# Optimization experiments

Hardware: AMD Instinct MI355X
Metric: run time of the kernel (lower is better)

The kernel has to match this reference:

```python
import jax, jax.numpy as jnp
import numpy as np

UNITS = 1024
NUM_HEADS = 16
MASK_VALUE = -1e12


def setup_inputs() -> dict:
    key = jax.random.key(0)
    k1, k2, k3, k4 = jax.random.split(key, 4)
    B, S = 8, 1024
    memory = jax.random.normal(k1, (B, S, 2 * UNITS), dtype=jnp.float32)
    query = jax.random.normal(k2, (B, S, UNITS), dtype=jnp.float32)
    b = jax.random.normal(k3, (S,), dtype=jnp.float32)
    seq_len = jax.random.randint(k4, (B, 1), 0, S, dtype=jnp.int32)
    return {"memory": memory, "query": query, "b": b, "seq_len": seq_len}


def _split_heads(x, n):
    # [B, S, D] -> [B, n, S, D/n]
    B, S, D = x.shape
    return x.reshape(B, S, n, D // n).transpose(0, 2, 1, 3)


def reference(memory, query, b, seq_len):
    B, S, _ = query.shape
    dh = UNITS // NUM_HEADS
    k_mem, v_mem = jnp.split(memory, 2, axis=2)
    Q = _split_heads(query, NUM_HEADS) * (dh ** -0.5)   # [B,H,S,dh]
    Kh = _split_heads(k_mem, NUM_HEADS)                  # [B,H,S,dh]
    Vh = _split_heads(v_mem, NUM_HEADS)                  # [B,H,S,dh]
    logits = jnp.einsum('bhqd,bhkd->bhqk', Q, Kh) + b    # bias broadcast over keys
    # mask: one_hot(seq_len) -> cumsum -> 1-cumsum == (pos < seq_len)
    valid = (jnp.arange(S)[None, :] < seq_len[:, 0:1]).astype(jnp.float32)  # [B,S]
    logits = logits + MASK_VALUE * (1.0 - valid)[:, None, None, :]
    weights = jax.nn.softmax(logits, axis=-1)
    out = jnp.einsum('bhqk,bhkd->bhqd', weights, Vh)
    return out.transpose(0, 2, 1, 3).reshape(B, S, UNITS)
```

## Files before the change

kernel.cpp:

```cpp
#include <hip/hip_runtime.h>
#include <hip/hip_bf16.h>

#define B_      8
#define S_      1024
#define H_      16
#define DH      64
#define UNITS_  1024
#define MSTRIDE 2048
#define KVB     64
#define QTB     64
#define LP      72

typedef __attribute__((ext_vector_type(8))) short bf16x8;
typedef __attribute__((ext_vector_type(4))) float f32x4;

__device__ __forceinline__ unsigned short f2bf(float f) {
    union { float f; unsigned u; } x; x.f = f;
    unsigned r = x.u + 0x7fffu + ((x.u >> 16) & 1u);
    return (unsigned short)(r >> 16);
}

__global__ __launch_bounds__(256)
void attn_kernel(const float* __restrict__ mem, const float* __restrict__ qry,
                 const float* __restrict__ bias, const int* __restrict__ slen,
                 float* __restrict__ out)
{
    __shared__ alignas(16) unsigned short Qs[QTB][LP];
    __shared__ alignas(16) unsigned short Ks[KVB][LP];
    __shared__ alignas(16) unsigned short Vt[DH][LP];
    __shared__ alignas(16) unsigned short Ps[4][16][LP];

    const int tid  = threadIdx.x;
    const int wq   = tid >> 6;
    const int lane = tid & 63;
    const int lr   = lane & 15;
    const int lg   = lane >> 4;

    const int qt = blockIdx.x;
    const int h  = blockIdx.y;
    const int b  = blockIdx.z;

    int L = slen[b];
    if (L == 0) L = S_;
    const int ntiles = (L + KVB - 1) / KVB;

    const float* qp = qry + ((size_t)(b * S_ + qt * QTB)) * UNITS_ + h * DH;
    const float* kp = mem + ((size_t)b * S_) * MSTRIDE + h * DH;
    const float* vp = kp + UNITS_;
    float*       op = out + ((size_t)(b * S_ + qt * QTB)) * UNITS_ + h * DH;

    {
        const int row = tid >> 2;
        const int cb  = (tid & 3) * 16;
        const float4* src = (const float4*)(qp + (size_t)row * UNITS_ + cb);
        union { unsigned short us[16]; uint4 v[2]; } t;
        #pragma unroll
        for (int i = 0; i < 4; ++i) {
            float4 f = src[i];
            t.us[i*4+0] = f2bf(f.x * 0.125f);
            t.us[i*4+1] = f2bf(f.y * 0.125f);
            t.us[i*4+2] = f2bf(f.z * 0.125f);
            t.us[i*4+3] = f2bf(f.w * 0.125f);
        }
        uint4* d = (uint4*)&Qs[row][cb];
        d[0] = t.v[0]; d[1] = t.v[1];
    }
    __syncthreads();

    bf16x8 qf[2];
    #pragma unroll
    for (int kc = 0; kc < 2; ++kc)
        qf[kc] = *(const bf16x8*)&Qs[wq*16 + lr][kc*32 + lg*8];

    f32x4 o[4];
    float m[4], ls[4];
    #pragma unroll
    for (int r = 0; r < 4; ++r) {
        o[r] = (f32x4){0.f,0.f,0.f,0.f};
        m[r] = -INFINITY; ls[r] = 0.f;
    }

    for (int t = 0; t < ntiles; ++t) {
        const int kvb = t * KVB;
        {
            const int row = tid >> 2;
            const int cb  = (tid & 3) * 16;
            const float4* ks = (const float4*)(kp + (size_t)(kvb + row) * MSTRIDE + cb);
            union { unsigned short us[16]; uint4 v[2]; } tk;
            #pragma unroll
            for (int i = 0; i < 4; ++i) {
                float4 f = ks[i];
                tk.us[i*4+0] = f2bf(f.x); tk.us[i*4+1] = f2bf(f.y);
                tk.us[i*4+2] = f2bf(f.z); tk.us[i*4+3] = f2bf(f.w);
            }
            uint4* d = (uint4*)&Ks[row][cb];
            d[0] = tk.v[0]; d[1] = tk.v[1];
            const float4* vs = (const float4*)(vp + (size_t)(kvb + row) * MSTRIDE + cb);
            #pragma unroll
            for (int i = 0; i < 4; ++i) {
                float4 f = vs[i];
                Vt[cb + i*4 + 0][row] = f2bf(f.x);
                Vt[cb + i*4 + 1][row] = f2bf(f.y);
                Vt[cb + i*4 + 2][row] = f2bf(f.z);
                Vt[cb + i*4 + 3][row] = f2bf(f.w);
            }
        }
        __syncthreads();

        f32x4 s[4];
        #pragma unroll
        for (int cb = 0; cb < 4; ++cb) {
            f32x4 acc = (f32x4){0.f,0.f,0.f,0.f};
            #pragma unroll
            for (int kc = 0; kc < 2; ++kc) {
                bf16x8 kf = *(const bf16x8*)&Ks[cb*16 + lr][kc*32 + lg*8];
                acc = __builtin_amdgcn_mfma_f32_16x16x32_bf16(qf[kc], kf, acc, 0, 0, 0);
            }
            s[cb] = acc;
        }

        float p[4][4];
        float rowm[4] = {-INFINITY, -INFINITY, -INFINITY, -INFINITY};
        #pragma unroll
        for (int cb = 0; cb < 4; ++cb) {
            const int key = kvb + cb*16 + lr;
            const float bb = bias[key];
            const bool valid = key < L;
            #pragma unroll
            for (int r = 0; r < 4; ++r) {
                float v = valid ? (s[cb][r] + bb) : -INFINITY;
                p[cb][r] = v;
                rowm[r] = fmaxf(rowm[r], v);
            }
        }
        #pragma unroll
        for (int off = 1; off < 16; off <<= 1) {
            #pragma unroll
            for (int r = 0; r < 4; ++r)
                rowm[r] = fmaxf(rowm[r], __shfl_xor(rowm[r], off, 64));
        }
        float sc[4], rs[4];
        #pragma unroll
        for (int r = 0; r < 4; ++r) {
            float mnew = fmaxf(m[r], rowm[r]);
            sc[r] = __expf(m[r] - mnew);
            m[r] = mnew;
            float acc = 0.f;
            #pragma unroll
            for (int cb = 0; cb < 4; ++cb) {
                float e = __expf(p[cb][r] - mnew);
                p[cb][r] = e;
                acc += e;
            }
            rs[r] = acc;
        }
        #pragma unroll
        for (int off = 1; off < 16; off <<= 1) {
            #pragma unroll
            for (int r = 0; r < 4; ++r)
                rs[r] += __shfl_xor(rs[r], off, 64);
        }
        #pragma unroll
        for (int r = 0; r < 4; ++r) {
            ls[r] = ls[r] * sc[r] + rs[r];
            #pragma unroll
            for (int c = 0; c < 4; ++c)
                o[c][r] *= sc[r];
        }

        #pragma unroll
        for (int cb = 0; cb < 4; ++cb)
            #pragma unroll
            for (int r = 0; r < 4; ++r)
                Ps[wq][lg*4 + r][cb*16 + lr] = f2bf(p[cb][r]);
        asm volatile("s_waitcnt lgkmcnt(0)" ::: "memory");

        #pragma unroll
        for (int kc = 0; kc < 2; ++kc) {
            bf16x8 pf = *(const bf16x8*)&Ps[wq][lr][kc*32 + lg*8];
            #pragma unroll
            for (int c = 0; c < 4; ++c) {
                bf16x8 vf = *(const bf16x8*)&Vt[c*16 + lr][kc*32 + lg*8];
                o[c] = __builtin_amdgcn_mfma_f32_16x16x32_bf16(pf, vf, o[c], 0, 0, 0);
            }
        }
        __syncthreads();
    }

    #pragma unroll
    for (int r = 0; r < 4; ++r) {
        const float inv = 1.0f / ls[r];
        float* orow = op + (size_t)(wq*16 + lg*4 + r) * UNITS_;
        #pragma unroll
        for (int c = 0; c < 4; ++c)
            orow[c*16 + lr] = o[c][r] * inv;
    }
}

extern "C" void kernel_launch(void* const* d_in, const int* in_sizes, int n_in,
                              void* d_out, int out_size, void* d_ws, size_t ws_size,
                              hipStream_t stream) {
    const float* mem  = (const float*)d_in[0];
    const float* qry  = (const float*)d_in[1];
    const float* bias = (const float*)d_in[2];
    const int*   slen = (const int*)d_in[3];
    float*       out  = (float*)d_out;
    dim3 grid(S_ / QTB, H_, B_);
    attn_kernel<<<grid, dim3(256), 0, stream>>>(mem, qry, bias, slen, out);
}
```

Before: 193.5 us.

## Double query rows per block, drop running max, use transposed LDS reads for V

```diff
diff --git a/kernel.cpp b/kernel.cpp
--- a/kernel.cpp
+++ b/kernel.cpp
@@ -1,5 +1,4 @@
 #include <hip/hip_runtime.h>
-#include <hip/hip_bf16.h>
 
 #define B_      8
 #define S_      1024
@@ -8,26 +7,27 @@
 #define UNITS_  1024
 #define MSTRIDE 2048
 #define KVB     64
-#define QTB     64
+#define QTB     128
 #define LP      72
+#define LOG2E   1.4426950408889634f
 
 typedef __attribute__((ext_vector_type(8))) short bf16x8;
+typedef __attribute__((ext_vector_type(4))) short bf16x4;
 typedef __attribute__((ext_vector_type(4))) float f32x4;
 
-__device__ __forceinline__ unsigned short f2bf(float f) {
-    union { float f; unsigned u; } x; x.f = f;
-    unsigned r = x.u + 0x7fffu + ((x.u >> 16) & 1u);
-    return (unsigned short)(r >> 16);
+__device__ __forceinline__ unsigned cvt_pk_bf16(float lo, float hi) {
+    unsigned r;
+    asm("v_cvt_pk_bf16_f32 %0, %1, %2" : "=v"(r) : "v"(lo), "v"(hi));
+    return r;
 }
 
-__global__ __launch_bounds__(256)
+__global__ __launch_bounds__(256, 4)
 void attn_kernel(const float* __restrict__ mem, const float* __restrict__ qry,
                  const float* __restrict__ bias, const int* __restrict__ slen,
                  float* __restrict__ out)
 {
-    __shared__ alignas(16) unsigned short Qs[QTB][LP];
     __shared__ alignas(16) unsigned short Ks[KVB][LP];
-    __shared__ alignas(16) unsigned short Vt[DH][LP];
+    __shared__ alignas(16) unsigned short Vs[KVB * DH];
     __shared__ alignas(16) unsigned short Ps[4][16][LP];
 
     const int tid  = threadIdx.x;
@@ -49,152 +49,143 @@
     const float* vp = kp + UNITS_;
     float*       op = out + ((size_t)(b * S_ + qt * QTB)) * UNITS_ + h * DH;
 
-    {
-        const int row = tid >> 2;
-        const int cb  = (tid & 3) * 16;
-        const float4* src = (const float4*)(qp + (size_t)row * UNITS_ + cb);
-        union { unsigned short us[16]; uint4 v[2]; } t;
-        #pragma unroll
-        for (int i = 0; i < 4; ++i) {
-            float4 f = src[i];
-            t.us[i*4+0] = f2bf(f.x * 0.125f);
-            t.us[i*4+1] = f2bf(f.y * 0.125f);
-            t.us[i*4+2] = f2bf(f.z * 0.125f);
-            t.us[i*4+3] = f2bf(f.w * 0.125f);
-        }
-        uint4* d = (uint4*)&Qs[row][cb];
-        d[0] = t.v[0]; d[1] = t.v[1];
-    }
-    __syncthreads();
-
-    bf16x8 qf[2];
+    bf16x8 qf[2][2];
     #pragma unroll
-    for (int kc = 0; kc < 2; ++kc)
-        qf[kc] = *(const bf16x8*)&Qs[wq*16 + lr][kc*32 + lg*8];
-
-    f32x4 o[4];
-    float m[4], ls[4];
+    for (int rb = 0; rb < 2; ++rb)
+      #pragma unroll
+      for (int kc = 0; kc < 2; ++kc) {
+        const float* qrow = qp + (size_t)(wq*32 + rb*16 + lr) * UNITS_ + kc*32 + lg*8;
+        float4 f0 = ((const float4*)qrow)[0];
+        float4 f1 = ((const float4*)qrow)[1];
+        const float sc = 0.125f * LOG2E;
+        uint4 u;
+        u.x = cvt_pk_bf16(f0.x*sc, f0.y*sc);
+        u.y = cvt_pk_bf16(f0.z*sc, f0.w*sc);
+        u.z = cvt_pk_bf16(f1.x*sc, f1.y*sc);
+        u.w = cvt_pk_bf16(f1.z*sc, f1.w*sc);
+        qf[rb][kc] = __builtin_bit_cast(bf16x8, u);
+      }
+
+    f32x4 o[2][4];
+    float ls[2][4];
     #pragma unroll
-    for (int r = 0; r < 4; ++r) {
-        o[r] = (f32x4){0.f,0.f,0.f,0.f};
-        m[r] = -INFINITY; ls[r] = 0.f;
-    }
+    for (int rb = 0; rb < 2; ++rb)
+      #pragma unroll
+      for (int r = 0; r < 4; ++r) {
+        o[rb][r] = (f32x4){0.f,0.f,0.f,0.f};
+        ls[rb][r] = 0.f;
+      }
+
+    const unsigned vsb = (unsigned)(uintptr_t)&Vs[0];
+    const int krow = tid >> 2;
+    const int dblk = tid & 3;
 
     for (int t = 0; t < ntiles; ++t) {
         const int kvb = t * KVB;
         {
-            const int row = tid >> 2;
-            const int cb  = (tid & 3) * 16;
-            const float4* ks = (const float4*)(kp + (size_t)(kvb + row) * MSTRIDE + cb);
-            union { unsigned short us[16]; uint4 v[2]; } tk;
+            const float4* ks = (const float4*)(kp + (size_t)(kvb + krow) * MSTRIDE + dblk * 16);
+            float4 a0 = ks[0], a1 = ks[1], a2 = ks[2], a3 = ks[3];
+            uint4 w0, w1;
+            w0.x = cvt_pk_bf16(a0.x, a0.y); w0.y = cvt_pk_bf16(a0.z, a0.w);
+            w0.z = cvt_pk_bf16(a1.x, a1.y); w0.w = cvt_pk_bf16(a1.z, a1.w);
+            w1.x = cvt_pk_bf16(a2.x, a2.y); w1.y = cvt_pk_bf16(a2.z, a2.w);
+            w1.z = cvt_pk_bf16(a3.x, a3.y); w1.w = cvt_pk_bf16(a3.z, a3.w);
+            uint4* d = (uint4*)&Ks[krow][dblk * 16];
+            d[0] = w0; d[1] = w1;
+        }
+        {
+            const float* vr = vp + (size_t)(kvb + krow) * MSTRIDE;
             #pragma unroll
             for (int i = 0; i < 4; ++i) {
-                float4 f = ks[i];
-                tk.us[i*4+0] = f2bf(f.x); tk.us[i*4+1] = f2bf(f.y);
-                tk.us[i*4+2] = f2bf(f.z); tk.us[i*4+3] = f2bf(f.w);
+                const int rot = (i + (krow >> 2)) & 3;
+                const int d0  = dblk * 16 + rot * 4;
+                float4 f = *(const float4*)(vr + d0);
+                uint2 w;
+                w.x = cvt_pk_bf16(f.x, f.y);
+                w.y = cvt_pk_bf16(f.z, f.w);
+                const int e = ((krow >> 2) << 8) + ((d0 >> 4) << 6) + ((krow & 3) << 4) + (d0 & 15);
+                *(uint2*)&Vs[e] = w;
             }
-            uint4* d = (uint4*)&Ks[row][cb];
-            d[0] = tk.v[0]; d[1] = tk.v[1];
-            const float4* vs = (const float4*)(vp + (size_t)(kvb + row) * MSTRIDE + cb);
-            #pragma unroll
-            for (int i = 0; i < 4; ++i) {
-                float4 f = vs[i];
-                Vt[cb + i*4 + 0][row] = f2bf(f.x);
-                Vt[cb + i*4 + 1][row] = f2bf(f.y);
-                Vt[cb + i*4 + 2][row] = f2bf(f.z);
-                Vt[cb + i*4 + 3][row] = f2bf(f.w);
+        }
+        __syncthreads();
+
+        float bv[4];
+        #pragma unroll
+        for (int cb = 0; cb < 4; ++cb) {
+            const int key = kvb + cb * 16 + lr;
+            bv[cb] = (key < L) ? bias[key] * LOG2E : -INFINITY;
+        }
+
+        bf16x4 vt[2][4][2];
+        #pragma unroll
+        for (int kc = 0; kc < 2; ++kc)
+          #pragma unroll
+          for (int c = 0; c < 4; ++c) {
+            unsigned a1 = vsb + ((kc * 8 + lg * 2) << 9) + (c << 7) + (lr << 3);
+            asm volatile("ds_read_b64_tr_b16 %0, %1" : "=v"(vt[kc][c][0]) : "v"(a1));
+            asm volatile("ds_read_b64_tr_b16 %0, %1 offset:512" : "=v"(vt[kc][c][1]) : "v"(a1));
+          }
+
+        #pragma unroll
+        for (int rb = 0; rb < 2; ++rb) {
+            f32x4 s[4];
+            #pragma unroll
+            for (int cb = 0; cb < 4; ++cb) {
+                f32x4 acc = (f32x4){0.f,0.f,0.f,0.f};
+                #pragma unroll
+                for (int kc = 0; kc < 2; ++kc) {
+                    bf16x8 kf = *(const bf16x8*)&Ks[cb * 16 + lr][kc * 32 + lg * 8];
+                    acc = __builtin_amdgcn_mfma_f32_16x16x32_bf16(qf[rb][kc], kf, acc, 0, 0, 0);
+                }
+                s[cb] = acc;
             }
-        }
-        __syncthreads();
-
-        f32x4 s[4];
-        #pragma unroll
-        for (int cb = 0; cb < 4; ++cb) {
-            f32x4 acc = (f32x4){0.f,0.f,0.f,0.f};
+            #pragma unroll
+            for (int cb = 0; cb < 4; ++cb)
+                #pragma unroll
+                for (int r = 0; r < 4; ++r) {
+                    float e = exp2f(s[cb][r] + bv[cb]);
+                    s[cb][r] = e;
+                    ls[rb][r] += e;
+                }
+            asm volatile("" ::: "memory");
+            #pragma unroll
+            for (int cb = 0; cb < 4; ++cb)
+                #pragma unroll
+                for (int r = 0; r < 4; r += 2) {
+                    unsigned u = cvt_pk_bf16(s[cb][r], s[cb][r + 1]);
+                    Ps[wq][lg * 4 + r][((cb ^ lg) & 3) * 16 + lr]     = (unsigned short)u;
+                    Ps[wq][lg * 4 + r + 1][((cb ^ lg) & 3) * 16 + lr] = (unsigned short)(u >> 16);
+                }
+            asm volatile("s_waitcnt lgkmcnt(0)" ::: "memory");
+            __builtin_amdgcn_sched_barrier(0);
             #pragma unroll
             for (int kc = 0; kc < 2; ++kc) {
-                bf16x8 kf = *(const bf16x8*)&Ks[cb*16 + lr][kc*32 + lg*8];
-                acc = __builtin_amdgcn_mfma_f32_16x16x32_bf16(qf[kc], kf, acc, 0, 0, 0);
-            }
-            s[cb] = acc;
-        }
-
-        float p[4][4];
-        float rowm[4] = {-INFINITY, -INFINITY, -INFINITY, -INFINITY};
-        #pragma unroll
-        for (int cb = 0; cb < 4; ++cb) {
-            const int key = kvb + cb*16 + lr;
-            const float bb = bias[key];
-            const bool valid = key < L;
-            #pragma unroll
-            for (int r = 0; r < 4; ++r) {
-                float v = valid ? (s[cb][r] + bb) : -INFINITY;
-                p[cb][r] = v;
-                rowm[r] = fmaxf(rowm[r], v);
-            }
-        }
-        #pragma unroll
-        for (int off = 1; off < 16; off <<= 1) {
-            #pragma unroll
-            for (int r = 0; r < 4; ++r)
-                rowm[r] = fmaxf(rowm[r], __shfl_xor(rowm[r], off, 64));
-        }
-        float sc[4], rs[4];
-        #pragma unroll
-        for (int r = 0; r < 4; ++r) {
-            float mnew = fmaxf(m[r], rowm[r]);
-            sc[r] = __expf(m[r] - mnew);
-            m[r] = mnew;
-            float acc = 0.f;
-            #pragma unroll
-            for (int cb = 0; cb < 4; ++cb) {
-                float e = __expf(p[cb][r] - mnew);
-                p[cb][r] = e;
-                acc += e;
-            }
-            rs[r] = acc;
-        }
-        #pragma unroll
-        for (int off = 1; off < 16; off <<= 1) {
-            #pragma unroll
-            for (int r = 0; r < 4; ++r)
-                rs[r] += __shfl_xor(rs[r], off, 64);
-        }
-        #pragma unroll
-        for (int r = 0; r < 4; ++r) {
-            ls[r] = ls[r] * sc[r] + rs[r];
-            #pragma unroll
-            for (int c = 0; c < 4; ++c)
-                o[c][r] *= sc[r];
-        }
-
-        #pragma unroll
-        for (int cb = 0; cb < 4; ++cb)
-            #pragma unroll
-            for (int r = 0; r < 4; ++r)
-                Ps[wq][lg*4 + r][cb*16 + lr] = f2bf(p[cb][r]);
-        asm volatile("s_waitcnt lgkmcnt(0)" ::: "memory");
-
-        #pragma unroll
-        for (int kc = 0; kc < 2; ++kc) {
-            bf16x8 pf = *(const bf16x8*)&Ps[wq][lr][kc*32 + lg*8];
-            #pragma unroll
-            for (int c = 0; c < 4; ++c) {
-                bf16x8 vf = *(const bf16x8*)&Vt[c*16 + lr][kc*32 + lg*8];
-                o[c] = __builtin_amdgcn_mfma_f32_16x16x32_bf16(pf, vf, o[c], 0, 0, 0);
+                bf16x8 pf = *(const bf16x8*)&Ps[wq][lr][((((kc * 2) + (lg >> 1)) ^ ((lr >> 2) & 3)) << 4) + ((lg & 1) << 3)];
+                #pragma unroll
+                for (int c = 0; c < 4; ++c) {
+                    bf16x8 vf = __builtin_shufflevector(vt[kc][c][0], vt[kc][c][1], 0,1,2,3,4,5,6,7);
+                    o[rb][c] = __builtin_amdgcn_mfma_f32_16x16x32_bf16(pf, vf, o[rb][c], 0, 0, 0);
+                }
             }
         }
         __syncthreads();
     }
 
     #pragma unroll
-    for (int r = 0; r < 4; ++r) {
-        const float inv = 1.0f / ls[r];
-        float* orow = op + (size_t)(wq*16 + lg*4 + r) * UNITS_;
-        #pragma unroll
-        for (int c = 0; c < 4; ++c)
-            orow[c*16 + lr] = o[c][r] * inv;
-    }
+    for (int rb = 0; rb < 2; ++rb)
+        #pragma unroll
+        for (int r = 0; r < 4; ++r) {
+            float v = ls[rb][r];
+            v += __shfl_xor(v, 1, 64);
+            v += __shfl_xor(v, 2, 64);
+            v += __shfl_xor(v, 4, 64);
+            v += __shfl_xor(v, 8, 64);
+            const float inv = 1.0f / v;
+            float* orow = op + (size_t)(wq * 32 + rb * 16 + lg * 4 + r) * UNITS_;
+            #pragma unroll
+            for (int c = 0; c < 4; ++c)
+                orow[c * 16 + lr] = o[rb][c][r] * inv;
+        }
 }
 
 extern "C" void kernel_launch(void* const* d_in, const int* in_sizes, int n_in,
```

New measurement: 230.3 us. 1.19x slower.
